# Kernel tuning notes

Measured on AMD Instinct MI355X. Metric: run time of the kernel, lower is better.

## Reference

```python
import jax, jax.numpy as jnp
import numpy as np

SIZE = 4096
N_ITER = 10
TEMP = 0.1


def setup_inputs() -> dict:
    key = jax.random.key(0)
    kx, kw = jax.random.split(key)
    x = jax.random.normal(kx, (4, 2048, SIZE), dtype=jnp.float32)
    weight = jax.random.normal(kw, (SIZE, SIZE), dtype=jnp.float32)
    r_prev = jnp.zeros((SIZE, 1), dtype=jnp.float32)
    c_prev = jnp.zeros((1, SIZE), dtype=jnp.float32)
    return {"x": x, "weight": weight, "r_prev": r_prev, "c_prev": c_prev}


def reference(x, weight, r_prev, c_prev):
    Q = weight / TEMP  # [S, S]

    def body(i, rc):
        r, c = rc
        r = -jax.nn.logsumexp(Q + c, axis=1, keepdims=True)  # [S, 1]
        c = -jax.nn.logsumexp(Q + r, axis=0, keepdims=True)  # [1, S]
        return (r, c)

    r, c = jax.lax.fori_loop(0, N_ITER, body, (r_prev, c_prev))
    P = jnp.exp(Q + r + c)  # doubly-stochastic-ish [S, S]
    # F.linear(x, P) == x @ P.T
    return jnp.einsum('btd,od->bto', x, P)
```

## Files before the change

kernel.cpp:

```cpp
#include <hip/hip_runtime.h>


#define L2E 1.44269504088896340736f

typedef __attribute__((ext_vector_type(8))) short bf16x8;
typedef __attribute__((ext_vector_type(4))) float f32x4;

__device__ __forceinline__ unsigned short f2bf(float x) {
  unsigned u = __float_as_uint(x);
  u += 0x7fffu + ((u >> 16) & 1u);
  return (unsigned short)(u >> 16);
}
__device__ __forceinline__ float bf2f(short x) {
  return __uint_as_float(((unsigned)(unsigned short)x) << 16);
}

__global__ void prep_e(const float* __restrict__ W, unsigned short* __restrict__ E) {
  const int row = blockIdx.x;
  const int t = threadIdx.x;
  const float* wp = W + ((size_t)row << 12);
  float v[16];
  float m = -3.4e38f;
#pragma unroll
  for (int ch = 0; ch < 4; ++ch) {
    float4 wv = *(const float4*)(wp + ch * 1024 + t * 4);
    float a0 = 10.f * wv.x, a1 = 10.f * wv.y, a2 = 10.f * wv.z, a3 = 10.f * wv.w;
    v[ch * 4 + 0] = a0; v[ch * 4 + 1] = a1; v[ch * 4 + 2] = a2; v[ch * 4 + 3] = a3;
    m = fmaxf(m, fmaxf(fmaxf(a0, a1), fmaxf(a2, a3)));
  }
#pragma unroll
  for (int off = 32; off > 0; off >>= 1) m = fmaxf(m, __shfl_xor(m, off));
  __shared__ float sm[4];
  if ((t & 63) == 0) sm[t >> 6] = m;
  __syncthreads();
  m = fmaxf(fmaxf(sm[0], sm[1]), fmaxf(sm[2], sm[3]));
  unsigned short* ep = E + ((size_t)row << 12);
#pragma unroll
  for (int ch = 0; ch < 4; ++ch) {
    ushort4 o;
    o.x = f2bf(exp2f((v[ch * 4 + 0] - m) * L2E));
    o.y = f2bf(exp2f((v[ch * 4 + 1] - m) * L2E));
    o.z = f2bf(exp2f((v[ch * 4 + 2] - m) * L2E));
    o.w = f2bf(exp2f((v[ch * 4 + 3] - m) * L2E));
    *(ushort4*)(ep + ch * 1024 + t * 4) = o;
  }
}

__global__ void transpose_bf(const unsigned short* __restrict__ E,
                             unsigned short* __restrict__ ET) {
  __shared__ unsigned short tile[64][66];
  const int t = threadIdx.x;
  const int r = t >> 3;
  const int c8 = (t & 7) << 3;
  const size_t i0 = (size_t)blockIdx.y << 6;
  const size_t j0 = (size_t)blockIdx.x << 6;
#pragma unroll
  for (int h = 0; h < 2; ++h) {
    bf16x8 vv = *(const bf16x8*)(E + (i0 + h * 32 + r) * 4096 + j0 + c8);
#pragma unroll
    for (int e = 0; e < 8; ++e) tile[h * 32 + r][c8 + e] = (unsigned short)vv[e];
  }
  __syncthreads();
#pragma unroll
  for (int h = 0; h < 2; ++h) {
    bf16x8 vv;
#pragma unroll
    for (int e = 0; e < 8; ++e) vv[e] = (short)tile[c8 + e][h * 32 + r];
    *(bf16x8*)(ET + (j0 + h * 32 + r) * 4096 + i0 + c8) = vv;
  }
}

__global__ void init_u(const float* __restrict__ c_prev, float* __restrict__ u) {
  const int i = blockIdx.x * 256 + threadIdx.x;
  u[i] = exp2f(c_prev[i] * L2E);
}

__global__ void recip_mv(const unsigned short* __restrict__ M,
                         const float* __restrict__ uin, float* __restrict__ vout) {
  const int t = threadIdx.x;
  const int l = t & 63, w = t >> 6;
  const int row = (blockIdx.x << 2) + w;
  const unsigned short* mp = M + ((size_t)row << 12);
  float s = 0.f;
#pragma unroll
  for (int ch = 0; ch < 8; ++ch) {
    const int j = (ch << 9) + (l << 3);
    bf16x8 e = *(const bf16x8*)(mp + j);
    const float4 u0 = *(const float4*)(uin + j);
    const float4 u1 = *(const float4*)(uin + j + 4);
    s = fmaf(bf2f(e[0]), u0.x, s);
    s = fmaf(bf2f(e[1]), u0.y, s);
    s = fmaf(bf2f(e[2]), u0.z, s);
    s = fmaf(bf2f(e[3]), u0.w, s);
    s = fmaf(bf2f(e[4]), u1.x, s);
    s = fmaf(bf2f(e[5]), u1.y, s);
    s = fmaf(bf2f(e[6]), u1.z, s);
    s = fmaf(bf2f(e[7]), u1.w, s);
  }
#pragma unroll
  for (int off = 32; off > 0; off >>= 1) s += __shfl_xor(s, off);
  if (l == 0) vout[row] = 1.f / s;
}

__global__ void scale_x(const float* __restrict__ X, const float* __restrict__ u,
                        unsigned short* __restrict__ Y) {
  const size_t idx = ((size_t)blockIdx.x * 256 + threadIdx.x) * 4;
  const int col = (int)(idx & 4095);
  float4 xv = *(const float4*)(X + idx);
  float4 uu = *(const float4*)(u + col);
  ushort4 o;
  o.x = f2bf(xv.x * uu.x);
  o.y = f2bf(xv.y * uu.y);
  o.z = f2bf(xv.z * uu.z);
  o.w = f2bf(xv.w * uu.w);
  *(ushort4*)(Y + idx) = o;
}

__global__ __launch_bounds__(512) void gemm_bt(const unsigned short* __restrict__ A,
                                               const unsigned short* __restrict__ B,
                                               const float* __restrict__ vscale,
                                               float* __restrict__ C) {
  __shared__ unsigned short lds[65536];
  const int t = threadIdx.x;
  const int l = t & 63;
  const int w = t >> 6;
  const int wm = w >> 2, wn = w & 3;

  int pid = blockIdx.x;
  pid = (pid & 7) * 64 + (pid >> 3);
  const int grp = pid >> 6;
  const int rem = pid & 63;
  const int bm = (grp << 2) + (rem & 3);
  const int bn = rem >> 2;
  const int m0 = bm << 8;
  const int n0 = bn << 8;

  const int ca = (((t & 3) ^ ((t >> 3) & 3)) << 3);
  const unsigned short* gA = A + (size_t)(m0 + (t >> 2)) * 4096 + ca;
  const unsigned short* gB = B + (size_t)(n0 + (t >> 2)) * 4096 + ca;

  const int xc = (((l >> 4) ^ ((l >> 1) & 3)) << 3);
  const int aOff = (wm * 128 + (l & 15)) * 32 + xc;
  const int bOff = (wn * 64 + (l & 15)) * 32 + xc;

  auto stageA = [&](int kt) {
    const int b = kt & 3;
    const unsigned short* g = gA + (size_t)kt * 32;
#pragma unroll
    for (int ra = 0; ra < 2; ++ra)
      __builtin_amdgcn_global_load_lds(
          (const __attribute__((address_space(1))) void*)(g + (size_t)ra * 524288),
          (__attribute__((address_space(3))) void*)((char*)lds + b * 16384 + ra * 8192 + w * 1024),
          16, 0, 0);
  };
  auto stageB = [&](int kt) {
    const int b = kt & 3;
    const unsigned short* g = gB + (size_t)kt * 32;
#pragma unroll
    for (int ra = 0; ra < 2; ++ra)
      __builtin_amdgcn_global_load_lds(
          (const __attribute__((address_space(1))) void*)(g + (size_t)ra * 524288),
          (__attribute__((address_space(3))) void*)((char*)lds + 65536 + b * 16384 + ra * 8192 + w * 1024),
          16, 0, 0);
  };

  f32x4 acc[8][4] = {};

  stageA(0); stageB(0);
  stageA(1); stageB(1);
  stageA(2); stageB(2);
  asm volatile("s_waitcnt vmcnt(8)" ::: "memory");
  __builtin_amdgcn_s_barrier();

  for (int kt = 0; kt < 128; ++kt) {
    const int buf = kt & 3;
    const unsigned short* aL = lds + buf * 8192 + aOff;
    const unsigned short* bL = lds + 32768 + buf * 8192 + bOff;
    bf16x8 afr[4], bfr[4];

#pragma unroll
    for (int i = 0; i < 4; ++i) afr[i] = *(const bf16x8*)(aL + i * 512);
#pragma unroll
    for (int j = 0; j < 4; ++j) bfr[j] = *(const bf16x8*)(bL + j * 512);
    if (kt < 125) stageA(kt + 3);
    __builtin_amdgcn_s_barrier();
    __builtin_amdgcn_s_setprio(1);
#pragma unroll
    for (int i = 0; i < 4; ++i)
#pragma unroll
      for (int j = 0; j < 4; ++j)
        acc[i][j] = __builtin_amdgcn_mfma_f32_16x16x32_bf16(afr[i], bfr[j], acc[i][j], 0, 0, 0);
    __builtin_amdgcn_s_setprio(0);
    __builtin_amdgcn_s_barrier();

#pragma unroll
    for (int i = 0; i < 4; ++i) afr[i] = *(const bf16x8*)(aL + (4 + i) * 512);
    if (kt < 125) stageB(kt + 3);
    __builtin_amdgcn_s_barrier();
    __builtin_amdgcn_s_setprio(1);
#pragma unroll
    for (int i = 0; i < 4; ++i)
#pragma unroll
      for (int j = 0; j < 4; ++j)
        acc[4 + i][j] = __builtin_amdgcn_mfma_f32_16x16x32_bf16(afr[i], bfr[j], acc[4 + i][j], 0, 0, 0);
    __builtin_amdgcn_s_setprio(0);

    if (kt < 125)        asm volatile("s_waitcnt vmcnt(8)" ::: "memory");
    else if (kt == 125)  asm volatile("s_waitcnt vmcnt(4)" ::: "memory");
    else if (kt == 126)  asm volatile("s_waitcnt vmcnt(0)" ::: "memory");
    __builtin_amdgcn_s_barrier();
  }

  const int crow = (l >> 4) << 2;
  const int ccol = l & 15;
#pragma unroll
  for (int j = 0; j < 4; ++j) {
    const int colj = n0 + (wn << 6) + (j << 4) + ccol;
    const float vs = vscale[colj];
#pragma unroll
    for (int i = 0; i < 8; ++i) {
      const int rowi = m0 + (wm << 7) + (i << 4) + crow;
#pragma unroll
      for (int q = 0; q < 4; ++q)
        C[((size_t)(rowi + q) << 12) + colj] = acc[i][j][q] * vs;
    }
  }
}

extern "C" void kernel_launch(void* const* d_in, const int* in_sizes, int n_in,
                              void* d_out, int out_size, void* d_ws, size_t ws_size,
                              hipStream_t stream) {
  const float* x      = (const float*)d_in[0];
  const float* weight = (const float*)d_in[1];
  const float* c_prev = (const float*)d_in[3];
  float* out = (float*)d_out;

  char* ws = (char*)d_ws;
  float* u = (float*)ws;
  float* v = (float*)(ws + (16 << 10));
  unsigned short* E  = (unsigned short*)(ws + (64 << 10));
  unsigned short* ET = E + (size_t)4096 * 4096;
  unsigned short* xb = ET;

  prep_e<<<4096, 256, 0, stream>>>(weight, E);
  transpose_bf<<<dim3(64, 64), 256, 0, stream>>>(E, ET);
  init_u<<<16, 256, 0, stream>>>(c_prev, u);

  for (int it = 0; it < 10; ++it) {
    recip_mv<<<1024, 256, 0, stream>>>(E, u, v);
    recip_mv<<<1024, 256, 0, stream>>>(ET, v, u);
  }

  scale_x<<<32768, 256, 0, stream>>>(x, u, xb);

  gemm_bt<<<512, 512, 0, stream>>>(xb, E, v, out);
}
```

Measured before the change: 449.1 us.

## Prefetch next k-tile LDS fragments across phases in GEMM main loop

Restructures the GEMM main loop so that the A and B register fragments for the next k-tile are read from LDS during the current tile's second phase, using a ping-pong register pair unrolled by two. The upper-half A fragments are loaded early in each phase. Waitcnt placement and sched_barriers are reordered so global-to-LDS staging overlaps the MFMA work. It also adds a launch-bounds occupancy hint of 2. The goal is to hide LDS read latency behind MFMAs, at the cost of higher register pressure and a more delicate wait/barrier ordering for buffer reuse.

```diff
diff --git a/kernel.cpp b/kernel.cpp
--- a/kernel.cpp
+++ b/kernel.cpp
@@ -116,10 +116,10 @@
   *(ushort4*)(Y + idx) = o;
 }
 
-__global__ __launch_bounds__(512) void gemm_bt(const unsigned short* __restrict__ A,
-                                               const unsigned short* __restrict__ B,
-                                               const float* __restrict__ vscale,
-                                               float* __restrict__ C) {
+__global__ __launch_bounds__(512, 2) void gemm_bt(const unsigned short* __restrict__ A,
+                                                  const unsigned short* __restrict__ B,
+                                                  const float* __restrict__ vscale,
+                                                  float* __restrict__ C) {
   __shared__ unsigned short lds[65536];
   const int t = threadIdx.x;
   const int l = t & 63;
@@ -172,44 +172,65 @@
   asm volatile("s_waitcnt vmcnt(8)" ::: "memory");
   __builtin_amdgcn_s_barrier();
 
-  for (int kt = 0; kt < 128; ++kt) {
-    const int buf = kt & 3;
-    const unsigned short* aL = lds + buf * 8192 + aOff;
-    const unsigned short* bL = lds + 32768 + buf * 8192 + bOff;
-    bf16x8 afr[4], bfr[4];
-
-#pragma unroll
-    for (int i = 0; i < 4; ++i) afr[i] = *(const bf16x8*)(aL + i * 512);
-#pragma unroll
-    for (int j = 0; j < 4; ++j) bfr[j] = *(const bf16x8*)(bL + j * 512);
-    if (kt < 125) stageA(kt + 3);
-    __builtin_amdgcn_s_barrier();
-    __builtin_amdgcn_s_setprio(1);
-#pragma unroll
-    for (int i = 0; i < 4; ++i)
-#pragma unroll
-      for (int j = 0; j < 4; ++j)
-        acc[i][j] = __builtin_amdgcn_mfma_f32_16x16x32_bf16(afr[i], bfr[j], acc[i][j], 0, 0, 0);
-    __builtin_amdgcn_s_setprio(0);
-    __builtin_amdgcn_s_barrier();
-
-#pragma unroll
-    for (int i = 0; i < 4; ++i) afr[i] = *(const bf16x8*)(aL + (4 + i) * 512);
-    if (kt < 125) stageB(kt + 3);
-    __builtin_amdgcn_s_barrier();
-    __builtin_amdgcn_s_setprio(1);
-#pragma unroll
-    for (int i = 0; i < 4; ++i)
-#pragma unroll
-      for (int j = 0; j < 4; ++j)
-        acc[4 + i][j] = __builtin_amdgcn_mfma_f32_16x16x32_bf16(afr[i], bfr[j], acc[4 + i][j], 0, 0, 0);
-    __builtin_amdgcn_s_setprio(0);
-
-    if (kt < 125)        asm volatile("s_waitcnt vmcnt(8)" ::: "memory");
-    else if (kt == 125)  asm volatile("s_waitcnt vmcnt(4)" ::: "memory");
-    else if (kt == 126)  asm volatile("s_waitcnt vmcnt(0)" ::: "memory");
-    __builtin_amdgcn_s_barrier();
-  }
+  bf16x8 cA[4], cB[4], nA[4], nB[4], hfr[4];
+#pragma unroll
+  for (int i = 0; i < 4; ++i) cA[i] = *(const bf16x8*)(lds + aOff + i * 512);
+#pragma unroll
+  for (int j = 0; j < 4; ++j) cB[j] = *(const bf16x8*)(lds + 32768 + bOff + j * 512);
+
+#define PHASE_PAIR(KT, CA, CB, NA, NB)                                            \
+  {                                                                               \
+    const int kt_ = (KT);                                                         \
+    const int buf_ = kt_ & 3;                                                     \
+    const unsigned short* aL = lds + buf_ * 8192 + aOff;                          \
+    const unsigned short* bL = lds + 32768 + buf_ * 8192 + bOff;                  \
+      \
+    _Pragma("unroll")                                                             \
+    for (int i = 0; i < 4; ++i) hfr[i] = *(const bf16x8*)(aL + (4 + i) * 512);    \
+    if (kt_ <= 124) stageA(kt_ + 3);                                              \
+    if (kt_ <= 124)      asm volatile("s_waitcnt vmcnt(6)" ::: "memory");         \
+    else if (kt_ == 125) asm volatile("s_waitcnt vmcnt(4)" ::: "memory");         \
+    else                 asm volatile("s_waitcnt vmcnt(0)" ::: "memory");         \
+    __builtin_amdgcn_sched_barrier(0);                                            \
+    __builtin_amdgcn_s_barrier();                                                 \
+    __builtin_amdgcn_s_setprio(1);                                                \
+    _Pragma("unroll")                                                             \
+    for (int i = 0; i < 4; ++i)                                                   \
+      _Pragma("unroll")                                                           \
+      for (int j = 0; j < 4; ++j)                                                 \
+        acc[i][j] = __builtin_amdgcn_mfma_f32_16x16x32_bf16(CA[i], CB[j],         \
+                                                            acc[i][j], 0, 0, 0); \
+    __builtin_amdgcn_s_setprio(0);                                                \
+    __builtin_amdgcn_s_barrier();                                                 \
+        \
+    if (kt_ <= 126) {                                                             \
+      const unsigned short* aN = lds + ((kt_ + 1) & 3) * 8192 + aOff;             \
+      const unsigned short* bN = lds + 32768 + ((kt_ + 1) & 3) * 8192 + bOff;     \
+      _Pragma("unroll")                                                           \
+      for (int i = 0; i < 4; ++i) NA[i] = *(const bf16x8*)(aN + i * 512);         \
+      _Pragma("unroll")                                                           \
+      for (int j = 0; j < 4; ++j) NB[j] = *(const bf16x8*)(bN + j * 512);         \
+    }                                                                             \
+    if (kt_ <= 124) stageB(kt_ + 3);                                              \
+    __builtin_amdgcn_sched_barrier(0);                                            \
+    __builtin_amdgcn_s_barrier();                                                 \
+    __builtin_amdgcn_s_setprio(1);                                                \
+    _Pragma("unroll")                                                             \
+    for (int i = 0; i < 4; ++i)                                                   \
+      _Pragma("unroll")                                                           \
+      for (int j = 0; j < 4; ++j)                                                 \
+        acc[4 + i][j] = __builtin_amdgcn_mfma_f32_16x16x32_bf16(hfr[i], CB[j],    \
+                                                                acc[4 + i][j],   \
+                                                                0, 0, 0);         \
+    __builtin_amdgcn_s_setprio(0);                                                \
+    __builtin_amdgcn_s_barrier();                                                 \
+  }
+
+  for (int kt = 0; kt < 128; kt += 2) {
+    PHASE_PAIR(kt, cA, cB, nA, nB)
+    PHASE_PAIR(kt + 1, nA, nB, cA, cB)
+  }
+#undef PHASE_PAIR
 
   const int crow = (l >> 4) << 2;
   const int ccol = l & 15;
```

New measurement: 444.9 us. No clear change (-0.9%).

## Unroll GEMM main loop over four LDS slots with shallower prefetch and occupancy hint

Applied to the files above, without the earlier changes.

The GEMM K-loop is unrolled by four stages so each LDS slot index is a compile-time constant, and the prefetch distance drops from three k-tiles to two. An explicit lgkmcnt wait plus a sched_barrier is added before each MFMA block. `__launch_bounds__(512, 2)` is also added to request two blocks per CU. The intent is to cut address arithmetic and give tighter control over scheduling. The risks are that the shallower prefetch exposes more global-load latency, and that the register cap implied by the occupancy hint may force the 128-register accumulator to spill.

```diff
diff --git a/kernel.cpp b/kernel.cpp
--- a/kernel.cpp
+++ b/kernel.cpp
@@ -116,10 +116,10 @@
   *(ushort4*)(Y + idx) = o;
 }
 
-__global__ __launch_bounds__(512) void gemm_bt(const unsigned short* __restrict__ A,
-                                               const unsigned short* __restrict__ B,
-                                               const float* __restrict__ vscale,
-                                               float* __restrict__ C) {
+__global__ __launch_bounds__(512, 2) void gemm_bt(const unsigned short* __restrict__ A,
+                                                  const unsigned short* __restrict__ B,
+                                                  const float* __restrict__ vscale,
+                                                  float* __restrict__ C) {
   __shared__ unsigned short lds[65536];
   const int t = threadIdx.x;
   const int l = t & 63;
@@ -140,76 +140,71 @@
   const unsigned short* gB = B + (size_t)(n0 + (t >> 2)) * 4096 + ca;
 
   const int xc = (((l >> 4) ^ ((l >> 1) & 3)) << 3);
-  const int aOff = (wm * 128 + (l & 15)) * 32 + xc;
-  const int bOff = (wn * 64 + (l & 15)) * 32 + xc;
-
-  auto stageA = [&](int kt) {
-    const int b = kt & 3;
-    const unsigned short* g = gA + (size_t)kt * 32;
+  const int aOff = wm * 4096 + (l & 15) * 32 + xc;
+  const int bOff = wn * 2048 + (l & 15) * 32 + xc;
+
+  auto stage = [&](const unsigned short* gbase, int h, int isB) {
+    const int slot = h & 3;
+    const unsigned short* g = gbase + (size_t)h * 32;
 #pragma unroll
     for (int ra = 0; ra < 2; ++ra)
       __builtin_amdgcn_global_load_lds(
           (const __attribute__((address_space(1))) void*)(g + (size_t)ra * 524288),
-          (__attribute__((address_space(3))) void*)((char*)lds + b * 16384 + ra * 8192 + w * 1024),
+          (__attribute__((address_space(3))) void*)((char*)lds + isB * 65536 + slot * 16384 + ra * 8192 + w * 1024),
           16, 0, 0);
   };
-  auto stageB = [&](int kt) {
-    const int b = kt & 3;
-    const unsigned short* g = gB + (size_t)kt * 32;
-#pragma unroll
-    for (int ra = 0; ra < 2; ++ra)
-      __builtin_amdgcn_global_load_lds(
-          (const __attribute__((address_space(1))) void*)(g + (size_t)ra * 524288),
-          (__attribute__((address_space(3))) void*)((char*)lds + 65536 + b * 16384 + ra * 8192 + w * 1024),
-          16, 0, 0);
-  };
 
   f32x4 acc[8][4] = {};
-
-  stageA(0); stageB(0);
-  stageA(1); stageB(1);
-  stageA(2); stageB(2);
-  asm volatile("s_waitcnt vmcnt(8)" ::: "memory");
+  bf16x8 afr[4], bfr[4];
+
+  stage(gA, 0, 0); stage(gB, 0, 1);
+  stage(gA, 1, 0); stage(gB, 1, 1);
+  asm volatile("s_waitcnt vmcnt(4)" ::: "memory");
   __builtin_amdgcn_s_barrier();
 
-  for (int kt = 0; kt < 128; ++kt) {
-    const int buf = kt & 3;
-    const unsigned short* aL = lds + buf * 8192 + aOff;
-    const unsigned short* bL = lds + 32768 + buf * 8192 + bOff;
-    bf16x8 afr[4], bfr[4];
-
-#pragma unroll
-    for (int i = 0; i < 4; ++i) afr[i] = *(const bf16x8*)(aL + i * 512);
-#pragma unroll
-    for (int j = 0; j < 4; ++j) bfr[j] = *(const bf16x8*)(bL + j * 512);
-    if (kt < 125) stageA(kt + 3);
-    __builtin_amdgcn_s_barrier();
-    __builtin_amdgcn_s_setprio(1);
-#pragma unroll
-    for (int i = 0; i < 4; ++i)
-#pragma unroll
-      for (int j = 0; j < 4; ++j)
-        acc[i][j] = __builtin_amdgcn_mfma_f32_16x16x32_bf16(afr[i], bfr[j], acc[i][j], 0, 0, 0);
-    __builtin_amdgcn_s_setprio(0);
-    __builtin_amdgcn_s_barrier();
-
-#pragma unroll
-    for (int i = 0; i < 4; ++i) afr[i] = *(const bf16x8*)(aL + (4 + i) * 512);
-    if (kt < 125) stageB(kt + 3);
-    __builtin_amdgcn_s_barrier();
-    __builtin_amdgcn_s_setprio(1);
-#pragma unroll
-    for (int i = 0; i < 4; ++i)
-#pragma unroll
-      for (int j = 0; j < 4; ++j)
-        acc[4 + i][j] = __builtin_amdgcn_mfma_f32_16x16x32_bf16(afr[i], bfr[j], acc[4 + i][j], 0, 0, 0);
-    __builtin_amdgcn_s_setprio(0);
-
-    if (kt < 125)        asm volatile("s_waitcnt vmcnt(8)" ::: "memory");
-    else if (kt == 125)  asm volatile("s_waitcnt vmcnt(4)" ::: "memory");
-    else if (kt == 126)  asm volatile("s_waitcnt vmcnt(0)" ::: "memory");
-    __builtin_amdgcn_s_barrier();
-  }
+#define PHASE(SLOT, MH, STAGE_STMT, WAIT_STMT)                                     \
+  {                                                                                \
+    const unsigned short* aL = lds + (SLOT) * 8192 + aOff + (MH) * 2048;           \
+    _Pragma("unroll")                                                              \
+    for (int i = 0; i < 4; ++i) afr[i] = *(const bf16x8*)(aL + i * 512);           \
+    if ((MH) == 0) {                                                               \
+      const unsigned short* bL = lds + 32768 + (SLOT) * 8192 + bOff;               \
+      _Pragma("unroll")                                                            \
+      for (int j = 0; j < 4; ++j) bfr[j] = *(const bf16x8*)(bL + j * 512);         \
+    }                                                                              \
+    STAGE_STMT;                                                                    \
+    __builtin_amdgcn_s_barrier();                                                  \
+    asm volatile("s_waitcnt lgkmcnt(0)" ::: "memory");                             \
+    __builtin_amdgcn_sched_barrier(0);                                             \
+    __builtin_amdgcn_s_setprio(1);                                                 \
+    _Pragma("unroll")                                                              \
+    for (int i = 0; i < 4; ++i)                                                    \
+      _Pragma("unroll")                                                            \
+      for (int j = 0; j < 4; ++j)                                                  \
+        acc[(MH) * 4 + i][j] = __builtin_amdgcn_mfma_f32_16x16x32_bf16(            \
+            afr[i], bfr[j], acc[(MH) * 4 + i][j], 0, 0, 0);                        \
+    __builtin_amdgcn_s_setprio(0);                                                 \
+    WAIT_STMT;                                                                     \
+    __builtin_amdgcn_s_barrier();                                                  \
+  }
+
+  for (int kt = 0; kt < 64; kt += 2) {
+    PHASE(0, 0, { if (kt <= 62) stage(gA, 2 * kt + 2, 0); }, {})
+    PHASE(0, 1, { if (kt <= 62) stage(gB, 2 * kt + 2, 1); },
+          { if (kt <= 62) asm volatile("s_waitcnt vmcnt(4)" ::: "memory");
+            else          asm volatile("s_waitcnt vmcnt(0)" ::: "memory"); })
+    PHASE(1, 0, { if (kt <= 62) stage(gA, 2 * kt + 3, 0); }, {})
+    PHASE(1, 1, { if (kt <= 62) stage(gB, 2 * kt + 3, 1); },
+          { if (kt <= 62) asm volatile("s_waitcnt vmcnt(4)" ::: "memory"); })
+    PHASE(2, 0, { if (kt + 1 <= 62) stage(gA, 2 * kt + 4, 0); }, {})
+    PHASE(2, 1, { if (kt + 1 <= 62) stage(gB, 2 * kt + 4, 1); },
+          { if (kt + 1 <= 62) asm volatile("s_waitcnt vmcnt(4)" ::: "memory");
+            else              asm volatile("s_waitcnt vmcnt(0)" ::: "memory"); })
+    PHASE(3, 0, { if (kt + 1 <= 62) stage(gA, 2 * kt + 5, 0); }, {})
+    PHASE(3, 1, { if (kt + 1 <= 62) stage(gB, 2 * kt + 5, 1); },
+          { if (kt + 1 <= 62) asm volatile("s_waitcnt vmcnt(4)" ::: "memory"); })
+  }
+#undef PHASE
 
   const int crow = (l >> 4) << 2;
   const int ccol = l & 15;
```

Result: faster. 436.4 us (-2.8%).

## Software-pipeline LDS fragment loads across GEMM k-steps with double-buffered B registers

Applied to the files above, without the earlier changes.

Restructures the bf16 GEMM main loop so the LDS reads for the next k-tile (A low half and B fragments) are issued during the current tile's second MFMA phase. B fragments are ping-ponged between two register sets, and fine-grained lgkmcnt/vmcnt waits with sched_barriers replace the coarser waits. The aim is to hide LDS read latency behind MFMA work. It also adds launch_bounds(512,2), which limits register use and could cause spills given the 128-register accumulator plus the extra fragment buffers.

```diff
diff --git a/kernel.cpp b/kernel.cpp
--- a/kernel.cpp
+++ b/kernel.cpp
@@ -116,10 +116,10 @@
   *(ushort4*)(Y + idx) = o;
 }
 
-__global__ __launch_bounds__(512) void gemm_bt(const unsigned short* __restrict__ A,
-                                               const unsigned short* __restrict__ B,
-                                               const float* __restrict__ vscale,
-                                               float* __restrict__ C) {
+__global__ __launch_bounds__(512, 2) void gemm_bt(const unsigned short* __restrict__ A,
+                                                  const unsigned short* __restrict__ B,
+                                                  const float* __restrict__ vscale,
+                                                  float* __restrict__ C) {
   __shared__ unsigned short lds[65536];
   const int t = threadIdx.x;
   const int l = t & 63;
@@ -165,51 +165,76 @@
   };
 
   f32x4 acc[8][4] = {};
+  bf16x8 aLo[4], aHi[4], Bc0[4], Bc1[4];
 
   stageA(0); stageB(0);
   stageA(1); stageB(1);
   stageA(2); stageB(2);
   asm volatile("s_waitcnt vmcnt(8)" ::: "memory");
   __builtin_amdgcn_s_barrier();
-
-  for (int kt = 0; kt < 128; ++kt) {
-    const int buf = kt & 3;
-    const unsigned short* aL = lds + buf * 8192 + aOff;
-    const unsigned short* bL = lds + 32768 + buf * 8192 + bOff;
-    bf16x8 afr[4], bfr[4];
-
-#pragma unroll
-    for (int i = 0; i < 4; ++i) afr[i] = *(const bf16x8*)(aL + i * 512);
-#pragma unroll
-    for (int j = 0; j < 4; ++j) bfr[j] = *(const bf16x8*)(bL + j * 512);
-    if (kt < 125) stageA(kt + 3);
-    __builtin_amdgcn_s_barrier();
-    __builtin_amdgcn_s_setprio(1);
-#pragma unroll
-    for (int i = 0; i < 4; ++i)
-#pragma unroll
-      for (int j = 0; j < 4; ++j)
-        acc[i][j] = __builtin_amdgcn_mfma_f32_16x16x32_bf16(afr[i], bfr[j], acc[i][j], 0, 0, 0);
-    __builtin_amdgcn_s_setprio(0);
-    __builtin_amdgcn_s_barrier();
-
-#pragma unroll
-    for (int i = 0; i < 4; ++i) afr[i] = *(const bf16x8*)(aL + (4 + i) * 512);
-    if (kt < 125) stageB(kt + 3);
-    __builtin_amdgcn_s_barrier();
-    __builtin_amdgcn_s_setprio(1);
-#pragma unroll
-    for (int i = 0; i < 4; ++i)
-#pragma unroll
-      for (int j = 0; j < 4; ++j)
-        acc[4 + i][j] = __builtin_amdgcn_mfma_f32_16x16x32_bf16(afr[i], bfr[j], acc[4 + i][j], 0, 0, 0);
-    __builtin_amdgcn_s_setprio(0);
-
-    if (kt < 125)        asm volatile("s_waitcnt vmcnt(8)" ::: "memory");
-    else if (kt == 125)  asm volatile("s_waitcnt vmcnt(4)" ::: "memory");
-    else if (kt == 126)  asm volatile("s_waitcnt vmcnt(0)" ::: "memory");
-    __builtin_amdgcn_s_barrier();
-  }
+#pragma unroll
+  for (int i = 0; i < 4; ++i) aLo[i] = *(const bf16x8*)(lds + aOff + i * 512);
+#pragma unroll
+  for (int j = 0; j < 4; ++j) Bc0[j] = *(const bf16x8*)(lds + 32768 + bOff + j * 512);
+
+#define MF(a, b, c) __builtin_amdgcn_mfma_f32_16x16x32_bf16(a, b, c, 0, 0, 0)
+
+#define P0(HV, BC)                                                             \
+  {                                                                            \
+    const unsigned short* aL = lds + ((HV) & 3) * 8192 + aOff;                 \
+    _Pragma("unroll")                                                          \
+    for (int i = 0; i < 4; ++i) aHi[i] = *(const bf16x8*)(aL + (4 + i) * 512); \
+    if ((HV) <= 124) stageA((HV) + 3);                                         \
+    if ((HV) <= 124)      asm volatile("s_waitcnt vmcnt(6)" ::: "memory");     \
+    else if ((HV) == 125) asm volatile("s_waitcnt vmcnt(4)" ::: "memory");     \
+    else if ((HV) == 126) asm volatile("s_waitcnt vmcnt(0)" ::: "memory");     \
+    __builtin_amdgcn_sched_barrier(0);                                         \
+    __builtin_amdgcn_s_barrier();                                              \
+    asm volatile("s_waitcnt lgkmcnt(4)" ::: "memory");                         \
+    __builtin_amdgcn_sched_barrier(0);                                         \
+    __builtin_amdgcn_s_setprio(1);                                             \
+    _Pragma("unroll")                                                          \
+    for (int i = 0; i < 4; ++i)                                                \
+      _Pragma("unroll")                                                        \
+      for (int j = 0; j < 4; ++j)                                              \
+        acc[i][j] = MF(aLo[i], BC[j], acc[i][j]);                              \
+    __builtin_amdgcn_s_setprio(0);                                             \
+    __builtin_amdgcn_s_barrier();                                              \
+  }
+
+#define P1(HV, BC, BN)                                                         \
+  {                                                                            \
+    if ((HV) <= 126) {                                                         \
+      const unsigned short* aN = lds + (((HV) + 1) & 3) * 8192 + aOff;         \
+      const unsigned short* bN = lds + 32768 + (((HV) + 1) & 3) * 8192 + bOff; \
+      _Pragma("unroll")                                                        \
+      for (int i = 0; i < 4; ++i) aLo[i] = *(const bf16x8*)(aN + i * 512);     \
+      _Pragma("unroll")                                                        \
+      for (int j = 0; j < 4; ++j) BN[j] = *(const bf16x8*)(bN + j * 512);      \
+    }                                                                          \
+    if ((HV) <= 124) stageB((HV) + 3);                                         \
+    __builtin_amdgcn_sched_barrier(0);                                         \
+    __builtin_amdgcn_s_barrier();                                              \
+    if ((HV) <= 126) asm volatile("s_waitcnt lgkmcnt(8)" ::: "memory");        \
+    else             asm volatile("s_waitcnt lgkmcnt(0)" ::: "memory");        \
+    __builtin_amdgcn_sched_barrier(0);                                         \
+    __builtin_amdgcn_s_setprio(1);                                             \
+    _Pragma("unroll")                                                          \
+    for (int i = 0; i < 4; ++i)                                                \
+      _Pragma("unroll")                                                        \
+      for (int j = 0; j < 4; ++j)                                              \
+        acc[4 + i][j] = MF(aHi[i], BC[j], acc[4 + i][j]);                      \
+    __builtin_amdgcn_s_setprio(0);                                             \
+    __builtin_amdgcn_s_barrier();                                              \
+  }
+
+  for (int h = 0; h < 128; h += 2) {
+    P0(h, Bc0) P1(h, Bc0, Bc1)
+    P0(h + 1, Bc1) P1(h + 1, Bc1, Bc0)
+  }
+#undef P0
+#undef P1
+#undef MF
 
   const int crow = (l >> 4) << 2;
   const int ccol = l & 15;
```

New measurement: 447.2 us. No clear change (-0.4%).
